# Kernel optimization log

Hardware: AMD Instinct MI355X
Metric: run time of the kernel (lower is better)

## Reference

```python
import jax, jax.numpy as jnp
import numpy as np

B, S, W = 16, 512, 5
H, E, V = 512, 256, 100000


def setup_inputs() -> dict:
    key = jax.random.key(0)
    ks = jax.random.split(key, 20)
    inp = {
        "hiddens": jax.random.normal(ks[0], (B, S, H), jnp.float32),
        "masks": jax.random.randint(ks[1], (B, S), 0, 2, jnp.int32),
        "begins": jax.random.randint(ks[2], (B, S, W), 0, V, jnp.int32),
        "begin_lens": jax.random.randint(ks[3], (B, S), 0, W + 1, jnp.int32),
        "middles": jax.random.randint(ks[4], (B, S, W), 0, V, jnp.int32),
        "middle_lens": jax.random.randint(ks[5], (B, S), 0, W + 1, jnp.int32),
        "ends": jax.random.randint(ks[6], (B, S, W), 0, V, jnp.int32),
        "end_lens": jax.random.randint(ks[7], (B, S), 0, W + 1, jnp.int32),
        # parameters
        "emb": jax.random.normal(ks[8], (V, E), jnp.float32) * 0.02,
        "W_hidden": jax.random.normal(ks[9], (H, 3 * H), jnp.float32) * (1.0 / np.sqrt(H)),
        "b_hidden": jnp.zeros((3 * H,), jnp.float32),
        "W_begin": jax.random.normal(ks[10], (E, 2 * H), jnp.float32) * (1.0 / np.sqrt(E)),
        "b_begin": jnp.zeros((2 * H,), jnp.float32),
        "W_middle": jax.random.normal(ks[11], (E, 2 * H), jnp.float32) * (1.0 / np.sqrt(E)),
        "b_middle": jnp.zeros((2 * H,), jnp.float32),
        "W_end": jax.random.normal(ks[12], (E, 2 * H), jnp.float32) * (1.0 / np.sqrt(E)),
        "b_end": jnp.zeros((2 * H,), jnp.float32),
        "W_gate": jax.random.normal(ks[13], (H, 9), jnp.float32) * (1.0 / np.sqrt(H)),
        "b_gate": jnp.zeros((9,), jnp.float32),
    }
    return inp


def _len_mask(lens, w):
    # True where the lattice candidate is valid (mimics _make_mask's 1s)
    return jnp.arange(w)[None, None, :] < lens[:, :, None]


def _gates(hiddens, masks, W_gate, b_gate):
    b, s, _ = hiddens.shape
    lmr = hiddens @ W_gate + b_gate                      # (B,S,9)
    left, mid, right = jnp.split(lmr, 3, axis=-1)        # each (B,S,3)
    g = jax.nn.sigmoid(left[:, :-2] + mid[:, 1:-1] + right[:, 2:])  # (B,S-2,3)
    ones = jnp.ones((b, 1), g.dtype)
    zeros = jnp.zeros((b, 1), g.dtype)
    begin_g = jnp.concatenate([ones, g[..., 0], ones], axis=1)
    mid_g = jnp.concatenate([zeros, g[..., 1], zeros], axis=1)
    end_g = jnp.concatenate([ones, g[..., 2], ones], axis=1)
    pad = masks == 0
    z = jnp.zeros((), g.dtype)
    return (jnp.where(pad, z, begin_g), jnp.where(pad, z, mid_g), jnp.where(pad, z, end_g))


def reference(hiddens, masks, begins, begin_lens, middles, middle_lens, ends, end_lens,
              emb, W_hidden, b_hidden, W_begin, b_begin, W_middle, b_middle,
              W_end, b_end, W_gate, b_gate):
    w = begins.shape[-1]
    begin_m = _len_mask(begin_lens, w)
    middle_m = _len_mask(middle_lens, w)
    end_m = _len_mask(end_lens, w)

    begin_kv = emb[begins] @ W_begin + b_begin           # (B,S,W,2H)
    middle_kv = emb[middles] @ W_middle + b_middle
    end_kv = emb[ends] @ W_end + b_end

    query, hidden_key, hidden_value = jnp.split(hiddens @ W_hidden + b_hidden, 3, axis=-1)
    bg, mg, eg = _gates(hiddens, masks, W_gate, b_gate)
    begin_kv = bg[:, :, None, None] * begin_kv
    middle_kv = mg[:, :, None, None] * middle_kv
    end_kv = eg[:, :, None, None] * end_kv

    kv = jnp.concatenate([begin_kv, middle_kv, end_kv], axis=-2)   # (B,S,3W,2H)
    h = hiddens.shape[-1]
    keys, values = jnp.split(kv, 2, axis=-1)
    keys = jnp.concatenate([hidden_key[:, :, None, :], keys], axis=-2)     # (B,S,1+3W,H)
    values = jnp.concatenate([hidden_value[:, :, None, :], values], axis=-2)

    # combined mask: True entries get -1e10 (faithful to masked_fill_(masks, -1e10))
    score_mask = jnp.concatenate(
        [(masks != 0)[:, :, None], begin_m, middle_m, end_m], axis=-1)     # (B,S,1+3W)

    scores = jnp.einsum("bsh,bskh->bsk", query, keys)
    scores = jnp.where(score_mask, jnp.asarray(-1e10, scores.dtype), scores)
    weights = jax.nn.softmax(scores, axis=-1)
    return jnp.einsum("bsk,bskh->bsh", weights, values)
```

## Files before the change

kernel.cpp:

```cpp
#include <hip/hip_runtime.h>
#include <cstdint>
#include <cstddef>


typedef unsigned short u16;
typedef __attribute__((ext_vector_type(8))) short short8;
typedef __attribute__((ext_vector_type(8))) __bf16 bf16x8;
typedef __attribute__((ext_vector_type(4))) float f32x4;

#define MROWS 8192
#define SS 512

static __device__ __forceinline__ u16 f2bf(float x) {
  uint32_t u = __builtin_bit_cast(uint32_t, x);
  u += 0x7FFFu + ((u >> 16) & 1u);
  return (u16)(u >> 16);
}
static __device__ __forceinline__ float bf2f(u16 h) {
  return __builtin_bit_cast(float, (uint32_t)h << 16);
}
static __device__ __forceinline__ float sigm(float x) { return 1.f / (1.f + __expf(-x)); }

__global__ void split_x_kernel(const float* __restrict__ X, u16* __restrict__ hi,
                               u16* __restrict__ lo, int n4) {
  int i = blockIdx.x * blockDim.x + threadIdx.x;
  if (i >= n4) return;
  float4 x = ((const float4*)X)[i];
  ushort4 h, l;
  h.x = f2bf(x.x); l.x = f2bf(x.x - bf2f(h.x));
  h.y = f2bf(x.y); l.y = f2bf(x.y - bf2f(h.y));
  h.z = f2bf(x.z); l.z = f2bf(x.z - bf2f(h.z));
  h.w = f2bf(x.w); l.w = f2bf(x.w - bf2f(h.w));
  ((ushort4*)hi)[i] = h;
  ((ushort4*)lo)[i] = l;
}

__global__ void transpose_split_wh(const float* __restrict__ Wsrc,
                                   u16* __restrict__ hi, u16* __restrict__ lo) {
  __shared__ float tile[64][65];
  int k0 = blockIdx.x * 64;
  int n0 = blockIdx.y * 64;
  int t = threadIdx.x;
#pragma unroll
  for (int i = 0; i < 16; i++) {
    int li = i * 256 + t; int r = li >> 6, c = li & 63;
    tile[r][c] = Wsrc[(size_t)(k0 + r) * 1536 + n0 + c];
  }
  __syncthreads();
#pragma unroll
  for (int i = 0; i < 16; i++) {
    int li = i * 256 + t; int r = li >> 6, c = li & 63;
    float v = tile[c][r];
    size_t o = (size_t)(n0 + r) * 512 + k0 + c;
    u16 h = f2bf(v);
    hi[o] = h;
    lo[o] = f2bf(v - bf2f(h));
  }
}

__global__ void build_wkT(const float* __restrict__ Wb, const float* __restrict__ Wm,
                          const float* __restrict__ We, const float* __restrict__ bb,
                          const float* __restrict__ bm, const float* __restrict__ be,
                          u16* __restrict__ WkT) {
  int tid = blockIdx.x * blockDim.x + threadIdx.x;
  if (tid >= 896 * 128) return;
  int n = tid >> 7;
  int kq = (tid & 127) * 4;
  float4 v;
  if (n < 768) {
    int ty = n >> 8, c = n & 255;
    const float* src = (ty == 0 ? Wb : ty == 1 ? Wm : We) + (size_t)c * 1024 + kq;
    v = *(const float4*)src;
  } else if (n < 771) {
    int ty = n - 768;
    const float* src = (ty == 0 ? bb : ty == 1 ? bm : be) + kq;
    v = *(const float4*)src;
  } else {
    v = make_float4(0.f, 0.f, 0.f, 0.f);
  }
  ushort4 h; h.x = f2bf(v.x); h.y = f2bf(v.y); h.z = f2bf(v.z); h.w = f2bf(v.w);
  ((ushort4*)WkT)[tid] = h;
}

__global__ void build_wvT(const float* __restrict__ Wb, const float* __restrict__ Wm,
                          const float* __restrict__ We, u16* __restrict__ WvT) {
  __shared__ float tile[64][65];
  int ty = blockIdx.z;
  const float* Wsrc = ty == 0 ? Wb : ty == 1 ? Wm : We;
  int c0 = blockIdx.x * 64;
  int n0 = blockIdx.y * 64;
  int t = threadIdx.x;
#pragma unroll
  for (int i = 0; i < 16; i++) {
    int li = i * 256 + t; int r = li >> 6, c = li & 63;
    tile[r][c] = Wsrc[(size_t)(c0 + r) * 1024 + 512 + n0 + c];
  }
  __syncthreads();
#pragma unroll
  for (int i = 0; i < 16; i++) {
    int li = i * 256 + t; int r = li >> 6, c = li & 63;
    float v = tile[c][r];
    WvT[(size_t)(n0 + r) * 768 + ty * 256 + c0 + c] = f2bf(v);
  }
}

__global__ __launch_bounds__(256) void lmr_kernel(const float* __restrict__ X,
                                                  const float* __restrict__ Wg,
                                                  const float* __restrict__ bg,
                                                  float* __restrict__ lmr) {
  __shared__ float wg[512 * 9];
  int t = threadIdx.x;
  for (int i = t; i < 4608; i += 256) wg[i] = Wg[i];
  __syncthreads();
  int lane = t & 63, wid = t >> 6;
  int pos = blockIdx.x * 4 + wid;
  const float* x = X + (size_t)pos * 512 + lane * 8;
  float4 x0 = *(const float4*)x;
  float4 x1 = *(const float4*)(x + 4);
  float xs[8] = {x0.x, x0.y, x0.z, x0.w, x1.x, x1.y, x1.z, x1.w};
  float p[9];
#pragma unroll
  for (int c = 0; c < 9; c++) p[c] = 0.f;
  const float* wrow = wg + (lane * 8) * 9;
#pragma unroll
  for (int j = 0; j < 8; j++)
#pragma unroll
    for (int c = 0; c < 9; c++) p[c] += xs[j] * wrow[j * 9 + c];
#pragma unroll
  for (int c = 0; c < 9; c++)
#pragma unroll
    for (int o = 32; o > 0; o >>= 1) p[c] += __shfl_xor(p[c], o);
  if (lane == 0) {
#pragma unroll
    for (int c = 0; c < 9; c++) lmr[(size_t)pos * 9 + c] = p[c] + bg[c];
  }
}

__global__ void gates_kernel(const float* __restrict__ lmr, const int* __restrict__ masks,
                             float* __restrict__ gates) {
  int pos = blockIdx.x * blockDim.x + threadIdx.x;
  if (pos >= MROWS) return;
  int s = pos & (SS - 1);
  float g0, g1, g2;
  if (masks[pos] == 0) {
    g0 = g1 = g2 = 0.f;
  } else if (s == 0 || s == SS - 1) {
    g0 = 1.f; g1 = 0.f; g2 = 1.f;
  } else {
    const float* l0 = lmr + (size_t)(pos - 1) * 9;
    const float* l1 = lmr + (size_t)pos * 9;
    const float* l2 = lmr + (size_t)(pos + 1) * 9;
    g0 = sigm(l0[0] + l1[3] + l2[6]);
    g1 = sigm(l0[1] + l1[4] + l2[7]);
    g2 = sigm(l0[2] + l1[5] + l2[8]);
  }
  gates[(size_t)pos * 3 + 0] = g0;
  gates[(size_t)pos * 3 + 1] = g1;
  gates[(size_t)pos * 3 + 2] = g2;
}

template <bool SPLIT, bool ADDOUT, bool WRITE_QBF, bool HAS_BIAS>
__global__ __launch_bounds__(256) void gemm_mfma(
    const u16* __restrict__ Ahi, const u16* __restrict__ Alo,
    const u16* __restrict__ Bhi, const u16* __restrict__ Blo,
    const float* __restrict__ bias, float* __restrict__ C, u16* __restrict__ Qbf,
    int Kdim, int ldC, int col0) {
  __shared__ __align__(16) u16 As_hi[128 * 32];
  __shared__ __align__(16) u16 Bs_hi[128 * 32];
  __shared__ __align__(16) u16 As_lo[SPLIT ? 128 * 32 : 8];
  __shared__ __align__(16) u16 Bs_lo[SPLIT ? 128 * 32 : 8];

  const int t = threadIdx.x;
  const int lane = t & 63;
  const int wid = t >> 6;
  const int m0 = blockIdx.x * 128;
  const int n0 = blockIdx.y * 128;
  const int wm = (wid & 1) * 64;
  const int wn = (wid >> 1) * 64;
  const int fr = lane & 15;
  const int kq = (lane >> 4) * 8;

  f32x4 acc[4][4];
#pragma unroll
  for (int i = 0; i < 4; i++)
#pragma unroll
    for (int j = 0; j < 4; j++) acc[i][j] = (f32x4){0.f, 0.f, 0.f, 0.f};

  for (int k0 = 0; k0 < Kdim; k0 += 32) {
    __syncthreads();
#pragma unroll
    for (int p = 0; p < 2; p++) {
      int li = p * 256 + t;
      int row = li >> 2;
      int so = (li & 3) * 8;
      size_t ga = (size_t)(m0 + row) * Kdim + k0 + so;
      size_t gb = (size_t)(n0 + row) * Kdim + k0 + so;
      int ls = row * 32 + so;
      *(uint4*)&As_hi[ls] = *(const uint4*)&Ahi[ga];
      *(uint4*)&Bs_hi[ls] = *(const uint4*)&Bhi[gb];
      if constexpr (SPLIT) {
        *(uint4*)&As_lo[ls] = *(const uint4*)&Alo[ga];
        *(uint4*)&Bs_lo[ls] = *(const uint4*)&Blo[gb];
      }
    }
    __syncthreads();
    short8 ah[4], bh[4], al[4], bl[4];
#pragma unroll
    for (int i = 0; i < 4; i++) {
      ah[i] = *(const short8*)&As_hi[(wm + i * 16 + fr) * 32 + kq];
      bh[i] = *(const short8*)&Bs_hi[(wn + i * 16 + fr) * 32 + kq];
      if constexpr (SPLIT) {
        al[i] = *(const short8*)&As_lo[(wm + i * 16 + fr) * 32 + kq];
        bl[i] = *(const short8*)&Bs_lo[(wn + i * 16 + fr) * 32 + kq];
      }
    }
#pragma unroll
    for (int mt = 0; mt < 4; mt++)
#pragma unroll
      for (int nt = 0; nt < 4; nt++) {
        acc[mt][nt] = __builtin_amdgcn_mfma_f32_16x16x32_bf16(
            __builtin_bit_cast(bf16x8, ah[mt]), __builtin_bit_cast(bf16x8, bh[nt]),
            acc[mt][nt], 0, 0, 0);
        if constexpr (SPLIT) {
          acc[mt][nt] = __builtin_amdgcn_mfma_f32_16x16x32_bf16(
              __builtin_bit_cast(bf16x8, al[mt]), __builtin_bit_cast(bf16x8, bh[nt]),
              acc[mt][nt], 0, 0, 0);
          acc[mt][nt] = __builtin_amdgcn_mfma_f32_16x16x32_bf16(
              __builtin_bit_cast(bf16x8, ah[mt]), __builtin_bit_cast(bf16x8, bl[nt]),
              acc[mt][nt], 0, 0, 0);
        }
      }
  }

  const int r0 = (lane >> 4) * 4;
#pragma unroll
  for (int mt = 0; mt < 4; mt++) {
#pragma unroll
    for (int nt = 0; nt < 4; nt++) {
      int col = col0 + n0 + wn + nt * 16 + fr;
      float bv = 0.f;
      if constexpr (HAS_BIAS) bv = bias[col];
#pragma unroll
      for (int r = 0; r < 4; r++) {
        int row = m0 + wm + mt * 16 + r0 + r;
        size_t off = (size_t)row * ldC + col;
        float v = acc[mt][nt][r] + bv;
        if constexpr (ADDOUT) v += C[off];
        C[off] = v;
        if constexpr (WRITE_QBF) {
          if (col < 512) Qbf[(size_t)row * 512 + col] = f2bf(v);
        }
      }
    }
  }
}

__global__ __launch_bounds__(256) void attn_kernel(
    const int* __restrict__ masks, const int* __restrict__ begins,
    const int* __restrict__ blens, const int* __restrict__ middles,
    const int* __restrict__ mlens, const int* __restrict__ ends,
    const int* __restrict__ elens, const float* __restrict__ emb,
    const float* __restrict__ QKV, const float* __restrict__ P,
    const float* __restrict__ gates, const float* __restrict__ b_begin,
    const float* __restrict__ b_middle, const float* __restrict__ b_end,
    float* __restrict__ out, u16* __restrict__ Ebar) {
  __shared__ float bvs[3][512];
  {
    int tt = threadIdx.x;
    for (int i = tt; i < 512; i += 256) {
      bvs[0][i] = b_begin[512 + i];
      bvs[1][i] = b_middle[512 + i];
      bvs[2][i] = b_end[512 + i];
    }
  }
  __syncthreads();
  const int t = threadIdx.x;
  const int lane = t & 63;
  const int wid = t >> 6;
  const int pos = blockIdx.x * 4 + wid;
  const int mask = masks[pos];
  const float* qkv = QKV + (size_t)pos * 1536;
  float4 hv0 = *(const float4*)(qkv + 1024 + lane * 8);
  float4 hv1 = *(const float4*)(qkv + 1024 + lane * 8 + 4);
  float* orow = out + (size_t)pos * 512;
  u16* erow = Ebar + (size_t)pos * 768;

  if (mask == 0) {
    float4 q0 = *(const float4*)(qkv + lane * 8);
    float4 q1 = *(const float4*)(qkv + lane * 8 + 4);
    float4 k0 = *(const float4*)(qkv + 512 + lane * 8);
    float4 k1 = *(const float4*)(qkv + 512 + lane * 8 + 4);
    float p = q0.x * k0.x + q0.y * k0.y + q0.z * k0.z + q0.w * k0.w +
              q1.x * k1.x + q1.y * k1.y + q1.z * k1.z + q1.w * k1.w;
#pragma unroll
    for (int o = 32; o > 0; o >>= 1) p += __shfl_xor(p, o);
    float s0 = p;
    int nv = min(blens[pos], 5) + min(mlens[pos], 5) + min(elens[pos], 5);
    int ninv = 15 - nv;
    float w0;
    if (ninv == 0) {
      w0 = 1.f;
    } else {
      float Mx = fmaxf(s0, 0.f);
      float e0 = __expf(s0 - Mx);
      w0 = e0 / (e0 + (float)ninv * __expf(-Mx));
    }
    float4 o0, o1;
    o0.x = w0 * hv0.x; o0.y = w0 * hv0.y; o0.z = w0 * hv0.z; o0.w = w0 * hv0.w;
    o1.x = w0 * hv1.x; o1.y = w0 * hv1.y; o1.z = w0 * hv1.z; o1.w = w0 * hv1.w;
    *(float4*)(orow + lane * 8) = o0;
    *(float4*)(orow + lane * 8 + 4) = o1;
    ushort4 zz; zz.x = zz.y = zz.z = zz.w = 0;
    *(ushort4*)(erow + 0 * 256 + lane * 4) = zz;
    *(ushort4*)(erow + 1 * 256 + lane * 4) = zz;
    *(ushort4*)(erow + 2 * 256 + lane * 4) = zz;
  } else {
    float g[3];
    g[0] = gates[(size_t)pos * 3 + 0];
    g[1] = gates[(size_t)pos * 3 + 1];
    g[2] = gates[(size_t)pos * 3 + 2];
    const float* prow = P + (size_t)pos * 896;
    float4 Pt[3];
    float qb[3];
#pragma unroll
    for (int ty = 0; ty < 3; ty++) {
      Pt[ty] = *(const float4*)(prow + ty * 256 + lane * 4);
      qb[ty] = prow[768 + ty];
    }
    int lens[3] = {blens[pos], mlens[pos], elens[pos]};
    const int* ib = begins + (size_t)pos * 5;
    const int* im = middles + (size_t)pos * 5;
    const int* ie = ends + (size_t)pos * 5;
    float4 ev[3][5];
#pragma unroll
    for (int w = 0; w < 5; w++) {
      ev[0][w] = *(const float4*)(emb + (size_t)ib[w] * 256 + lane * 4);
      ev[1][w] = *(const float4*)(emb + (size_t)im[w] * 256 + lane * 4);
      ev[2][w] = *(const float4*)(emb + (size_t)ie[w] * 256 + lane * 4);
    }
    float sc[16];
    sc[0] = -1e10f;
#pragma unroll
    for (int ty = 0; ty < 3; ty++) {
#pragma unroll
      for (int w = 0; w < 5; w++) {
        float4 e = ev[ty][w];
        float d = Pt[ty].x * e.x + Pt[ty].y * e.y + Pt[ty].z * e.z + Pt[ty].w * e.w;
#pragma unroll
        for (int o = 32; o > 0; o >>= 1) d += __shfl_xor(d, o);
        sc[1 + ty * 5 + w] = (w < lens[ty]) ? -1e10f : g[ty] * (d + qb[ty]);
      }
    }
    float Mx = sc[0];
#pragma unroll
    for (int k = 1; k < 16; k++) Mx = fmaxf(Mx, sc[k]);
    float wts[16];
    float zs = 0.f;
#pragma unroll
    for (int k = 0; k < 16; k++) {
      wts[k] = __expf(sc[k] - Mx);
      zs += wts[k];
    }
    float inv = 1.f / zs;
    float alpha[3];
#pragma unroll
    for (int ty = 0; ty < 3; ty++) {
      float ax = 0.f, ay = 0.f, az = 0.f, aw = 0.f, asum = 0.f;
#pragma unroll
      for (int w = 0; w < 5; w++) {
        float wk = wts[1 + ty * 5 + w];
        asum += wk;
        ax += wk * ev[ty][w].x;
        ay += wk * ev[ty][w].y;
        az += wk * ev[ty][w].z;
        aw += wk * ev[ty][w].w;
      }
      float sg = g[ty] * inv;
      alpha[ty] = sg * asum;
      ushort4 h;
      h.x = f2bf(ax * sg); h.y = f2bf(ay * sg); h.z = f2bf(az * sg); h.w = f2bf(aw * sg);
      *(ushort4*)(erow + ty * 256 + lane * 4) = h;
    }
    float w0 = wts[0] * inv;
    float4 o0, o1;
    int hb = lane * 8;
    o0.x = w0 * hv0.x + alpha[0] * bvs[0][hb + 0] + alpha[1] * bvs[1][hb + 0] + alpha[2] * bvs[2][hb + 0];
    o0.y = w0 * hv0.y + alpha[0] * bvs[0][hb + 1] + alpha[1] * bvs[1][hb + 1] + alpha[2] * bvs[2][hb + 1];
    o0.z = w0 * hv0.z + alpha[0] * bvs[0][hb + 2] + alpha[1] * bvs[1][hb + 2] + alpha[2] * bvs[2][hb + 2];
    o0.w = w0 * hv0.w + alpha[0] * bvs[0][hb + 3] + alpha[1] * bvs[1][hb + 3] + alpha[2] * bvs[2][hb + 3];
    o1.x = w0 * hv1.x + alpha[0] * bvs[0][hb + 4] + alpha[1] * bvs[1][hb + 4] + alpha[2] * bvs[2][hb + 4];
    o1.y = w0 * hv1.y + alpha[0] * bvs[0][hb + 5] + alpha[1] * bvs[1][hb + 5] + alpha[2] * bvs[2][hb + 5];
    o1.z = w0 * hv1.z + alpha[0] * bvs[0][hb + 6] + alpha[1] * bvs[1][hb + 6] + alpha[2] * bvs[2][hb + 6];
    o1.w = w0 * hv1.w + alpha[0] * bvs[0][hb + 7] + alpha[1] * bvs[1][hb + 7] + alpha[2] * bvs[2][hb + 7];
    *(float4*)(orow + lane * 8) = o0;
    *(float4*)(orow + lane * 8 + 4) = o1;
  }
}

extern "C" void kernel_launch(void* const* d_in, const int* in_sizes, int n_in,
                              void* d_out, int out_size, void* d_ws, size_t ws_size,
                              hipStream_t stream) {
  const float* hiddens = (const float*)d_in[0];
  const int* masks = (const int*)d_in[1];
  const int* begins = (const int*)d_in[2];
  const int* blens = (const int*)d_in[3];
  const int* middles = (const int*)d_in[4];
  const int* mlens = (const int*)d_in[5];
  const int* ends = (const int*)d_in[6];
  const int* elens = (const int*)d_in[7];
  const float* emb = (const float*)d_in[8];
  const float* Wh = (const float*)d_in[9];
  const float* bh = (const float*)d_in[10];
  const float* Wb = (const float*)d_in[11];
  const float* bb = (const float*)d_in[12];
  const float* Wm = (const float*)d_in[13];
  const float* bm = (const float*)d_in[14];
  const float* We = (const float*)d_in[15];
  const float* be = (const float*)d_in[16];
  const float* Wg = (const float*)d_in[17];
  const float* bg = (const float*)d_in[18];
  float* out = (float*)d_out;

  char* ws = (char*)d_ws;
  size_t off = 0;
  auto alloc = [&](size_t bytes) -> char* {
    char* p = ws + off;
    off += (bytes + 255) & ~(size_t)255;
    return p;
  };
  u16* Xhi = (u16*)alloc((size_t)8192 * 512 * 2);
  u16* Xlo = (u16*)alloc((size_t)8192 * 512 * 2);
  u16* WhThi = (u16*)alloc((size_t)1536 * 512 * 2);
  u16* WhTlo = (u16*)alloc((size_t)1536 * 512 * 2);
  u16* WkT = (u16*)alloc((size_t)896 * 512 * 2);
  u16* WvT = (u16*)alloc((size_t)512 * 768 * 2);
  float* QKV = (float*)alloc((size_t)8192 * 1536 * 4);
  u16* Qbf = (u16*)alloc((size_t)8192 * 512 * 2);
  float* P = (float*)alloc((size_t)8192 * 896 * 4);
  float* lmr = (float*)alloc((size_t)8192 * 9 * 4);
  float* gates = (float*)alloc((size_t)8192 * 3 * 4);
  u16* Ebar = (u16*)alloc((size_t)8192 * 768 * 2);
  if (off > ws_size) return;

  split_x_kernel<<<4096, 256, 0, stream>>>(hiddens, Xhi, Xlo, 1048576);
  transpose_split_wh<<<dim3(8, 24), 256, 0, stream>>>(Wh, WhThi, WhTlo);
  build_wkT<<<448, 256, 0, stream>>>(Wb, Wm, We, bb, bm, be, WkT);
  build_wvT<<<dim3(4, 8, 3), 256, 0, stream>>>(Wb, Wm, We, WvT);
  lmr_kernel<<<2048, 256, 0, stream>>>(hiddens, Wg, bg, lmr);
  gates_kernel<<<32, 256, 0, stream>>>(lmr, masks, gates);

  gemm_mfma<true, false, true, true><<<dim3(64, 8), 256, 0, stream>>>(
      Xhi, Xlo, WhThi, WhTlo, bh, QKV, Qbf, 512, 1536, 0);
  gemm_mfma<false, false, false, true><<<dim3(64, 4), 256, 0, stream>>>(
      Xhi, nullptr, WhThi + (size_t)1024 * 512, nullptr, bh, QKV, nullptr, 512, 1536, 1024);

  gemm_mfma<false, false, false, false><<<dim3(64, 7), 256, 0, stream>>>(
      Qbf, nullptr, WkT, nullptr, nullptr, P, nullptr, 512, 896, 0);

  attn_kernel<<<2048, 256, 0, stream>>>(masks, begins, blens, middles, mlens, ends,
                                        elens, emb, QKV, P, gates, bb, bm, be, out, Ebar);

  gemm_mfma<false, true, false, false><<<dim3(64, 4), 256, 0, stream>>>(
      Ebar, nullptr, WvT, nullptr, nullptr, out, nullptr, 768, 512, 0);
}
```

Measured before the change: 328.0 us.

## Fuse prep kernels, merge QKV GEMMs, use direct LDS loads, store P in bf16

Six small setup kernels become two. One converts hiddens to hi/lo bf16 while also computing the gate logits; the other builds all weight layouts and the gates, selected by block index. The two QKV GEMM launches become one, with a runtime flag that uses the split-precision path only for the query/key columns. GEMM tiles now go straight from global memory to LDS via global_load_lds, and the P projection is written as bf16 instead of fp32, halving its traffic into the attention kernel. The aim is fewer launches and less memory traffic, at the cost of lower precision in the scores and a runtime branch inside the GEMM.

```diff
diff --git a/kernel.cpp b/kernel.cpp
--- a/kernel.cpp
+++ b/kernel.cpp
@@ -21,160 +21,164 @@
 }
 static __device__ __forceinline__ float sigm(float x) { return 1.f / (1.f + __expf(-x)); }
 
-__global__ void split_x_kernel(const float* __restrict__ X, u16* __restrict__ hi,
-                               u16* __restrict__ lo, int n4) {
-  int i = blockIdx.x * blockDim.x + threadIdx.x;
-  if (i >= n4) return;
-  float4 x = ((const float4*)X)[i];
-  ushort4 h, l;
-  h.x = f2bf(x.x); l.x = f2bf(x.x - bf2f(h.x));
-  h.y = f2bf(x.y); l.y = f2bf(x.y - bf2f(h.y));
-  h.z = f2bf(x.z); l.z = f2bf(x.z - bf2f(h.z));
-  h.w = f2bf(x.w); l.w = f2bf(x.w - bf2f(h.w));
-  ((ushort4*)hi)[i] = h;
-  ((ushort4*)lo)[i] = l;
-}
-
-__global__ void transpose_split_wh(const float* __restrict__ Wsrc,
-                                   u16* __restrict__ hi, u16* __restrict__ lo) {
-  __shared__ float tile[64][65];
-  int k0 = blockIdx.x * 64;
-  int n0 = blockIdx.y * 64;
-  int t = threadIdx.x;
-#pragma unroll
-  for (int i = 0; i < 16; i++) {
-    int li = i * 256 + t; int r = li >> 6, c = li & 63;
-    tile[r][c] = Wsrc[(size_t)(k0 + r) * 1536 + n0 + c];
-  }
-  __syncthreads();
-#pragma unroll
-  for (int i = 0; i < 16; i++) {
-    int li = i * 256 + t; int r = li >> 6, c = li & 63;
-    float v = tile[c][r];
-    size_t o = (size_t)(n0 + r) * 512 + k0 + c;
-    u16 h = f2bf(v);
-    hi[o] = h;
-    lo[o] = f2bf(v - bf2f(h));
-  }
-}
-
-__global__ void build_wkT(const float* __restrict__ Wb, const float* __restrict__ Wm,
-                          const float* __restrict__ We, const float* __restrict__ bb,
-                          const float* __restrict__ bm, const float* __restrict__ be,
-                          u16* __restrict__ WkT) {
-  int tid = blockIdx.x * blockDim.x + threadIdx.x;
-  if (tid >= 896 * 128) return;
-  int n = tid >> 7;
-  int kq = (tid & 127) * 4;
-  float4 v;
-  if (n < 768) {
-    int ty = n >> 8, c = n & 255;
-    const float* src = (ty == 0 ? Wb : ty == 1 ? Wm : We) + (size_t)c * 1024 + kq;
-    v = *(const float4*)src;
-  } else if (n < 771) {
-    int ty = n - 768;
-    const float* src = (ty == 0 ? bb : ty == 1 ? bm : be) + kq;
-    v = *(const float4*)src;
-  } else {
-    v = make_float4(0.f, 0.f, 0.f, 0.f);
-  }
-  ushort4 h; h.x = f2bf(v.x); h.y = f2bf(v.y); h.z = f2bf(v.z); h.w = f2bf(v.w);
-  ((ushort4*)WkT)[tid] = h;
-}
-
-__global__ void build_wvT(const float* __restrict__ Wb, const float* __restrict__ Wm,
-                          const float* __restrict__ We, u16* __restrict__ WvT) {
-  __shared__ float tile[64][65];
-  int ty = blockIdx.z;
-  const float* Wsrc = ty == 0 ? Wb : ty == 1 ? Wm : We;
-  int c0 = blockIdx.x * 64;
-  int n0 = blockIdx.y * 64;
-  int t = threadIdx.x;
-#pragma unroll
-  for (int i = 0; i < 16; i++) {
-    int li = i * 256 + t; int r = li >> 6, c = li & 63;
-    tile[r][c] = Wsrc[(size_t)(c0 + r) * 1024 + 512 + n0 + c];
-  }
-  __syncthreads();
-#pragma unroll
-  for (int i = 0; i < 16; i++) {
-    int li = i * 256 + t; int r = li >> 6, c = li & 63;
-    float v = tile[c][r];
-    WvT[(size_t)(n0 + r) * 768 + ty * 256 + c0 + c] = f2bf(v);
-  }
-}
-
-__global__ __launch_bounds__(256) void lmr_kernel(const float* __restrict__ X,
-                                                  const float* __restrict__ Wg,
-                                                  const float* __restrict__ bg,
-                                                  float* __restrict__ lmr) {
-  __shared__ float wg[512 * 9];
-  int t = threadIdx.x;
+static __device__ __forceinline__ void gl2lds(const u16* g, u16* l) {
+  __builtin_amdgcn_global_load_lds(
+      (const __attribute__((address_space(1))) unsigned int*)g,
+      (__attribute__((address_space(3))) unsigned int*)l, 16, 0, 0);
+}
+
+__global__ __launch_bounds__(256) void prep_xlmr(
+    const float* __restrict__ X, const float* __restrict__ Wg,
+    const float* __restrict__ bg, u16* __restrict__ hi, u16* __restrict__ lo,
+    float* __restrict__ lmr) {
+  __shared__ float wg[4608];
+  const int t = threadIdx.x;
   for (int i = t; i < 4608; i += 256) wg[i] = Wg[i];
   __syncthreads();
-  int lane = t & 63, wid = t >> 6;
-  int pos = blockIdx.x * 4 + wid;
-  const float* x = X + (size_t)pos * 512 + lane * 8;
-  float4 x0 = *(const float4*)x;
-  float4 x1 = *(const float4*)(x + 4);
-  float xs[8] = {x0.x, x0.y, x0.z, x0.w, x1.x, x1.y, x1.z, x1.w};
-  float p[9];
-#pragma unroll
-  for (int c = 0; c < 9; c++) p[c] = 0.f;
-  const float* wrow = wg + (lane * 8) * 9;
-#pragma unroll
-  for (int j = 0; j < 8; j++)
-#pragma unroll
-    for (int c = 0; c < 9; c++) p[c] += xs[j] * wrow[j * 9 + c];
-#pragma unroll
-  for (int c = 0; c < 9; c++)
-#pragma unroll
-    for (int o = 32; o > 0; o >>= 1) p[c] += __shfl_xor(p[c], o);
-  if (lane == 0) {
-#pragma unroll
-    for (int c = 0; c < 9; c++) lmr[(size_t)pos * 9 + c] = p[c] + bg[c];
-  }
-}
-
-__global__ void gates_kernel(const float* __restrict__ lmr, const int* __restrict__ masks,
-                             float* __restrict__ gates) {
-  int pos = blockIdx.x * blockDim.x + threadIdx.x;
-  if (pos >= MROWS) return;
-  int s = pos & (SS - 1);
-  float g0, g1, g2;
-  if (masks[pos] == 0) {
-    g0 = g1 = g2 = 0.f;
-  } else if (s == 0 || s == SS - 1) {
-    g0 = 1.f; g1 = 0.f; g2 = 1.f;
+  const int lane = t & 63, wid = t >> 6;
+#pragma unroll
+  for (int it = 0; it < 4; it++) {
+    int pos = blockIdx.x * 16 + it * 4 + wid;
+    const float* x = X + (size_t)pos * 512 + lane * 8;
+    float4 x0 = *(const float4*)x;
+    float4 x1 = *(const float4*)(x + 4);
+    float xs[8] = {x0.x, x0.y, x0.z, x0.w, x1.x, x1.y, x1.z, x1.w};
+    ushort4 h0, h1, l0, l1;
+    h0.x = f2bf(xs[0]); l0.x = f2bf(xs[0] - bf2f(h0.x));
+    h0.y = f2bf(xs[1]); l0.y = f2bf(xs[1] - bf2f(h0.y));
+    h0.z = f2bf(xs[2]); l0.z = f2bf(xs[2] - bf2f(h0.z));
+    h0.w = f2bf(xs[3]); l0.w = f2bf(xs[3] - bf2f(h0.w));
+    h1.x = f2bf(xs[4]); l1.x = f2bf(xs[4] - bf2f(h1.x));
+    h1.y = f2bf(xs[5]); l1.y = f2bf(xs[5] - bf2f(h1.y));
+    h1.z = f2bf(xs[6]); l1.z = f2bf(xs[6] - bf2f(h1.z));
+    h1.w = f2bf(xs[7]); l1.w = f2bf(xs[7] - bf2f(h1.w));
+    ((ushort4*)hi)[pos * 128 + lane * 2] = h0;
+    ((ushort4*)hi)[pos * 128 + lane * 2 + 1] = h1;
+    ((ushort4*)lo)[pos * 128 + lane * 2] = l0;
+    ((ushort4*)lo)[pos * 128 + lane * 2 + 1] = l1;
+    float p[9];
+#pragma unroll
+    for (int c = 0; c < 9; c++) p[c] = 0.f;
+    const float* wrow = wg + (lane * 8) * 9;
+#pragma unroll
+    for (int j = 0; j < 8; j++)
+#pragma unroll
+      for (int c = 0; c < 9; c++) p[c] += xs[j] * wrow[j * 9 + c];
+#pragma unroll
+    for (int c = 0; c < 9; c++)
+#pragma unroll
+      for (int o = 32; o > 0; o >>= 1) p[c] += __shfl_xor(p[c], o);
+    if (lane == 0) {
+#pragma unroll
+      for (int c = 0; c < 9; c++) lmr[(size_t)pos * 9 + c] = p[c] + bg[c];
+    }
+  }
+}
+
+__global__ __launch_bounds__(256) void prep_weights(
+    const float* __restrict__ Wh, const float* __restrict__ Wb,
+    const float* __restrict__ Wm, const float* __restrict__ We,
+    const float* __restrict__ bb, const float* __restrict__ bm,
+    const float* __restrict__ be, const float* __restrict__ lmr,
+    const int* __restrict__ masks, u16* __restrict__ WhThi,
+    u16* __restrict__ WhTlo, u16* __restrict__ WkT, u16* __restrict__ WvT,
+    float* __restrict__ gates) {
+  __shared__ float tile[64][65];
+  const int b = blockIdx.x;
+  const int t = threadIdx.x;
+  if (b < 192) {
+    int k0 = (b & 7) * 64;
+    int n0 = (b >> 3) * 64;
+#pragma unroll
+    for (int i = 0; i < 16; i++) {
+      int li = i * 256 + t; int r = li >> 6, c = li & 63;
+      tile[r][c] = Wh[(size_t)(k0 + r) * 1536 + n0 + c];
+    }
+    __syncthreads();
+#pragma unroll
+    for (int i = 0; i < 16; i++) {
+      int li = i * 256 + t; int r = li >> 6, c = li & 63;
+      float v = tile[c][r];
+      size_t o = (size_t)(n0 + r) * 512 + k0 + c;
+      u16 h = f2bf(v);
+      WhThi[o] = h;
+      WhTlo[o] = f2bf(v - bf2f(h));
+    }
+  } else if (b < 640) {
+    int tid = (b - 192) * 256 + t;
+    int n = tid >> 7;
+    int kq = (tid & 127) * 4;
+    float4 v;
+    if (n < 768) {
+      int ty = n >> 8, c = n & 255;
+      const float* src = (ty == 0 ? Wb : ty == 1 ? Wm : We) + (size_t)c * 1024 + kq;
+      v = *(const float4*)src;
+    } else if (n < 771) {
+      int ty = n - 768;
+      const float* src = (ty == 0 ? bb : ty == 1 ? bm : be) + kq;
+      v = *(const float4*)src;
+    } else {
+      v = make_float4(0.f, 0.f, 0.f, 0.f);
+    }
+    ushort4 h; h.x = f2bf(v.x); h.y = f2bf(v.y); h.z = f2bf(v.z); h.w = f2bf(v.w);
+    ((ushort4*)WkT)[tid] = h;
+  } else if (b < 736) {
+    int idx = b - 640;
+    int ty = idx >> 5;
+    int rem = idx & 31;
+    int c0 = (rem & 3) * 64;
+    int n0 = (rem >> 2) * 64;
+    const float* Wsrc = ty == 0 ? Wb : ty == 1 ? Wm : We;
+#pragma unroll
+    for (int i = 0; i < 16; i++) {
+      int li = i * 256 + t; int r = li >> 6, c = li & 63;
+      tile[r][c] = Wsrc[(size_t)(c0 + r) * 1024 + 512 + n0 + c];
+    }
+    __syncthreads();
+#pragma unroll
+    for (int i = 0; i < 16; i++) {
+      int li = i * 256 + t; int r = li >> 6, c = li & 63;
+      WvT[(size_t)(n0 + r) * 768 + ty * 256 + c0 + c] = f2bf(tile[c][r]);
+    }
   } else {
-    const float* l0 = lmr + (size_t)(pos - 1) * 9;
-    const float* l1 = lmr + (size_t)pos * 9;
-    const float* l2 = lmr + (size_t)(pos + 1) * 9;
-    g0 = sigm(l0[0] + l1[3] + l2[6]);
-    g1 = sigm(l0[1] + l1[4] + l2[7]);
-    g2 = sigm(l0[2] + l1[5] + l2[8]);
-  }
-  gates[(size_t)pos * 3 + 0] = g0;
-  gates[(size_t)pos * 3 + 1] = g1;
-  gates[(size_t)pos * 3 + 2] = g2;
-}
-
-template <bool SPLIT, bool ADDOUT, bool WRITE_QBF, bool HAS_BIAS>
+    int pos = (b - 736) * 256 + t;
+    int s = pos & (SS - 1);
+    float g0, g1, g2;
+    if (masks[pos] == 0) {
+      g0 = g1 = g2 = 0.f;
+    } else if (s == 0 || s == SS - 1) {
+      g0 = 1.f; g1 = 0.f; g2 = 1.f;
+    } else {
+      const float* p0 = lmr + (size_t)(pos - 1) * 9;
+      const float* p1 = lmr + (size_t)pos * 9;
+      const float* p2 = lmr + (size_t)(pos + 1) * 9;
+      g0 = sigm(p0[0] + p1[3] + p2[6]);
+      g1 = sigm(p0[1] + p1[4] + p2[7]);
+      g2 = sigm(p0[2] + p1[5] + p2[8]);
+    }
+    gates[(size_t)pos * 3 + 0] = g0;
+    gates[(size_t)pos * 3 + 1] = g1;
+    gates[(size_t)pos * 3 + 2] = g2;
+  }
+}
+
+template <bool MAYSPLIT, bool ADDOUT, bool WRITE_QBF, bool HAS_BIAS, bool OUTBF>
 __global__ __launch_bounds__(256) void gemm_mfma(
     const u16* __restrict__ Ahi, const u16* __restrict__ Alo,
     const u16* __restrict__ Bhi, const u16* __restrict__ Blo,
-    const float* __restrict__ bias, float* __restrict__ C, u16* __restrict__ Qbf,
-    int Kdim, int ldC, int col0) {
+    const float* __restrict__ bias, float* __restrict__ Cf, u16* __restrict__ Cb,
+    u16* __restrict__ Qbf, int Kdim, int ldC, int splitN) {
   __shared__ __align__(16) u16 As_hi[128 * 32];
   __shared__ __align__(16) u16 Bs_hi[128 * 32];
-  __shared__ __align__(16) u16 As_lo[SPLIT ? 128 * 32 : 8];
-  __shared__ __align__(16) u16 Bs_lo[SPLIT ? 128 * 32 : 8];
+  __shared__ __align__(16) u16 As_lo[MAYSPLIT ? 128 * 32 : 8];
+  __shared__ __align__(16) u16 Bs_lo[MAYSPLIT ? 128 * 32 : 8];
 
   const int t = threadIdx.x;
   const int lane = t & 63;
   const int wid = t >> 6;
   const int m0 = blockIdx.x * 128;
   const int n0 = blockIdx.y * 128;
+  const bool split = MAYSPLIT && (n0 < splitN);
   const int wm = (wid & 1) * 64;
   const int wn = (wid >> 1) * 64;
   const int fr = lane & 15;
@@ -195,12 +199,12 @@
       int so = (li & 3) * 8;
       size_t ga = (size_t)(m0 + row) * Kdim + k0 + so;
       size_t gb = (size_t)(n0 + row) * Kdim + k0 + so;
-      int ls = row * 32 + so;
-      *(uint4*)&As_hi[ls] = *(const uint4*)&Ahi[ga];
-      *(uint4*)&Bs_hi[ls] = *(const uint4*)&Bhi[gb];
-      if constexpr (SPLIT) {
-        *(uint4*)&As_lo[ls] = *(const uint4*)&Alo[ga];
-        *(uint4*)&Bs_lo[ls] = *(const uint4*)&Blo[gb];
+      int ls = li * 8;
+      gl2lds(&Ahi[ga], &As_hi[ls]);
+      gl2lds(&Bhi[gb], &Bs_hi[ls]);
+      if (MAYSPLIT && split) {
+        gl2lds(&Alo[ga], &As_lo[ls]);
+        gl2lds(&Blo[gb], &Bs_lo[ls]);
       }
     }
     __syncthreads();
@@ -209,7 +213,7 @@
     for (int i = 0; i < 4; i++) {
       ah[i] = *(const short8*)&As_hi[(wm + i * 16 + fr) * 32 + kq];
       bh[i] = *(const short8*)&Bs_hi[(wn + i * 16 + fr) * 32 + kq];
-      if constexpr (SPLIT) {
+      if (MAYSPLIT && split) {
         al[i] = *(const short8*)&As_lo[(wm + i * 16 + fr) * 32 + kq];
         bl[i] = *(const short8*)&Bs_lo[(wn + i * 16 + fr) * 32 + kq];
       }
@@ -221,7 +225,7 @@
         acc[mt][nt] = __builtin_amdgcn_mfma_f32_16x16x32_bf16(
             __builtin_bit_cast(bf16x8, ah[mt]), __builtin_bit_cast(bf16x8, bh[nt]),
             acc[mt][nt], 0, 0, 0);
-        if constexpr (SPLIT) {
+        if (MAYSPLIT && split) {
           acc[mt][nt] = __builtin_amdgcn_mfma_f32_16x16x32_bf16(
               __builtin_bit_cast(bf16x8, al[mt]), __builtin_bit_cast(bf16x8, bh[nt]),
               acc[mt][nt], 0, 0, 0);
@@ -237,7 +241,7 @@
   for (int mt = 0; mt < 4; mt++) {
 #pragma unroll
     for (int nt = 0; nt < 4; nt++) {
-      int col = col0 + n0 + wn + nt * 16 + fr;
+      int col = n0 + wn + nt * 16 + fr;
       float bv = 0.f;
       if constexpr (HAS_BIAS) bv = bias[col];
 #pragma unroll
@@ -245,8 +249,9 @@
         int row = m0 + wm + mt * 16 + r0 + r;
         size_t off = (size_t)row * ldC + col;
         float v = acc[mt][nt][r] + bv;
-        if constexpr (ADDOUT) v += C[off];
-        C[off] = v;
+        if constexpr (ADDOUT) v += Cf[off];
+        if constexpr (OUTBF) Cb[off] = f2bf(v);
+        else Cf[off] = v;
         if constexpr (WRITE_QBF) {
           if (col < 512) Qbf[(size_t)row * 512 + col] = f2bf(v);
         }
@@ -260,7 +265,7 @@
     const int* __restrict__ blens, const int* __restrict__ middles,
     const int* __restrict__ mlens, const int* __restrict__ ends,
     const int* __restrict__ elens, const float* __restrict__ emb,
-    const float* __restrict__ QKV, const float* __restrict__ P,
+    const float* __restrict__ QKV, const u16* __restrict__ Pb,
     const float* __restrict__ gates, const float* __restrict__ b_begin,
     const float* __restrict__ b_middle, const float* __restrict__ b_end,
     float* __restrict__ out, u16* __restrict__ Ebar) {
@@ -319,13 +324,15 @@
     g[0] = gates[(size_t)pos * 3 + 0];
     g[1] = gates[(size_t)pos * 3 + 1];
     g[2] = gates[(size_t)pos * 3 + 2];
-    const float* prow = P + (size_t)pos * 896;
+    const u16* prow = Pb + (size_t)pos * 896;
     float4 Pt[3];
     float qb[3];
 #pragma unroll
     for (int ty = 0; ty < 3; ty++) {
-      Pt[ty] = *(const float4*)(prow + ty * 256 + lane * 4);
-      qb[ty] = prow[768 + ty];
+      ushort4 pu = *(const ushort4*)(prow + ty * 256 + lane * 4);
+      Pt[ty].x = bf2f(pu.x); Pt[ty].y = bf2f(pu.y);
+      Pt[ty].z = bf2f(pu.z); Pt[ty].w = bf2f(pu.w);
+      qb[ty] = bf2f(prow[768 + ty]);
     }
     int lens[3] = {blens[pos], mlens[pos], elens[pos]};
     const int* ib = begins + (size_t)pos * 5;
@@ -436,30 +443,21 @@
   u16* WvT = (u16*)alloc((size_t)512 * 768 * 2);
   float* QKV = (float*)alloc((size_t)8192 * 1536 * 4);
   u16* Qbf = (u16*)alloc((size_t)8192 * 512 * 2);
-  float* P = (float*)alloc((size_t)8192 * 896 * 4);
+  u16* Pb = (u16*)alloc((size_t)8192 * 896 * 2);
   float* lmr = (float*)alloc((size_t)8192 * 9 * 4);
   float* gates = (float*)alloc((size_t)8192 * 3 * 4);
   u16* Ebar = (u16*)alloc((size_t)8192 * 768 * 2);
   if (off > ws_size) return;
 
-  split_x_kernel<<<4096, 256, 0, stream>>>(hiddens, Xhi, Xlo, 1048576);
-  transpose_split_wh<<<dim3(8, 24), 256, 0, stream>>>(Wh, WhThi, WhTlo);
-  build_wkT<<<448, 256, 0, stream>>>(Wb, Wm, We, bb, bm, be, WkT);
-  build_wvT<<<dim3(4, 8, 3), 256, 0, stream>>>(Wb, Wm, We, WvT);
-  lmr_kernel<<<2048, 256, 0, stream>>>(hiddens, Wg, bg, lmr);
-  gates_kernel<<<32, 256, 0, stream>>>(lmr, masks, gates);
-
-  gemm_mfma<true, false, true, true><<<dim3(64, 8), 256, 0, stream>>>(
-      Xhi, Xlo, WhThi, WhTlo, bh, QKV, Qbf, 512, 1536, 0);
-  gemm_mfma<false, false, false, true><<<dim3(64, 4), 256, 0, stream>>>(
-      Xhi, nullptr, WhThi + (size_t)1024 * 512, nullptr, bh, QKV, nullptr, 512, 1536, 1024);
-
-  gemm_mfma<false, false, false, false><<<dim3(64, 7), 256, 0, stream>>>(
-      Qbf, nullptr, WkT, nullptr, nullptr, P, nullptr, 512, 896, 0);
-
+  prep_xlmr<<<512, 256, 0, stream>>>(hiddens, Wg, bg, Xhi, Xlo, lmr);
+  prep_weights<<<768, 256, 0, stream>>>(Wh, Wb, Wm, We, bb, bm, be, lmr, masks,
+                                        WhThi, WhTlo, WkT, WvT, gates);
+  gemm_mfma<true, false, true, true, false><<<dim3(64, 12), 256, 0, stream>>>(
+      Xhi, Xlo, WhThi, WhTlo, bh, QKV, nullptr, Qbf, 512, 1536, 1024);
+  gemm_mfma<false, false, false, false, true><<<dim3(64, 7), 256, 0, stream>>>(
+      Qbf, nullptr, WkT, nullptr, nullptr, nullptr, Pb, nullptr, 512, 896, 0);
   attn_kernel<<<2048, 256, 0, stream>>>(masks, begins, blens, middles, mlens, ends,
-                                        elens, emb, QKV, P, gates, bb, bm, be, out, Ebar);
-
-  gemm_mfma<false, true, false, false><<<dim3(64, 4), 256, 0, stream>>>(
-      Ebar, nullptr, WvT, nullptr, nullptr, out, nullptr, 768, 512, 0);
-}
+                                        elens, emb, QKV, Pb, gates, bb, bm, be, out, Ebar);
+  gemm_mfma<false, true, false, false, false><<<dim3(64, 4), 256, 0, stream>>>(
+      Ebar, nullptr, WvT, nullptr, nullptr, out, nullptr, nullptr, 768, 512, 0);
+}
```

New measurement: 315.8 us. -3.7%, faster.
